# Kernel optimization log

Measured on AMD Instinct MI355X. Metric: run time of the kernel, lower is better.

## Reference

```python
import jax, jax.numpy as jnp
import numpy as np

C = 512
HEADS = 8
HEAD_DIM = C // HEADS
GROUPS = 32
EPS = 1e-5


def group_norm(x, scale, bias):
    b, c, h, w = x.shape
    xg = x.reshape(b, GROUPS, -1)
    mean = xg.mean(axis=-1, keepdims=True)
    var = xg.var(axis=-1, keepdims=True)
    xg = (xg - mean) * jax.lax.rsqrt(var + EPS)
    x = xg.reshape(b, c, h, w)
    return x * scale[None, :, None, None] + bias[None, :, None, None]


def conv1x1(x, w, b):
    # w: (out_c, in_c), x: (B, C, H, W)
    return jnp.einsum('oc,bchw->bohw', w, x) + b[None, :, None, None]


def setup_inputs() -> dict:
    key = jax.random.key(0)
    ks = jax.random.split(key, 11)
    s = 1.0 / np.sqrt(C)
    return {
        'x': jax.random.normal(ks[0], (8, C, 32, 32), jnp.float32),
        'gn_scale': jnp.ones((C,), jnp.float32),
        'gn_bias': jnp.zeros((C,), jnp.float32),
        'wq': jax.random.normal(ks[1], (C, C), jnp.float32) * s,
        'bq': jax.random.normal(ks[2], (C,), jnp.float32) * 0.01,
        'wk': jax.random.normal(ks[3], (C, C), jnp.float32) * s,
        'bk': jax.random.normal(ks[4], (C,), jnp.float32) * 0.01,
        'wv': jax.random.normal(ks[5], (C, C), jnp.float32) * s,
        'bv': jax.random.normal(ks[6], (C,), jnp.float32) * 0.01,
        'wp': jax.random.normal(ks[7], (C, C), jnp.float32) * s,
        'bp': jax.random.normal(ks[8], (C,), jnp.float32) * 0.01,
    }


def reference(x, gn_scale, gn_bias, wq, bq, wk, bk, wv, bv, wp, bp):
    b, c, h, w = x.shape
    n = h * w
    h_in = x
    xn = group_norm(x, gn_scale, gn_bias)
    q = conv1x1(xn, wq, bq).reshape(b, HEADS, HEAD_DIM, n)
    k = conv1x1(xn, wk, bk).reshape(b, HEADS, HEAD_DIM, n)
    v = conv1x1(xn, wv, bv).reshape(b, HEADS, HEAD_DIM, n)
    scale = 1.0 / np.sqrt(HEAD_DIM).astype(np.float32)
    attn = jnp.einsum('bhcn,bhcm->bhnm', q, k) * scale
    attn = jax.nn.softmax(attn, axis=-1)
    out = jnp.einsum('bhnm,bhcm->bhcn', attn, v)
    out = out.reshape(b, c, h, w)
    out = conv1x1(out, wp, bp)
    return out + h_in
```

## Files before the change

kernel.cpp:

```cpp
#include <hip/hip_runtime.h>

#define CC 512
#define NN 1024
#define NB 8
#define NH 8
#define HD 64

typedef __attribute__((ext_vector_type(8))) short s16x8;
typedef __attribute__((ext_vector_type(4))) short s16x4;
typedef __attribute__((ext_vector_type(4))) float f32x4;
typedef __attribute__((ext_vector_type(16))) float f32x16;

__device__ __forceinline__ unsigned cvtpk(float lo, float hi){
  unsigned r;
  asm("v_cvt_pk_bf16_f32 %0, %1, %2" : "=v"(r) : "v"(lo), "v"(hi));
  return r;
}

__device__ __forceinline__ s16x4 pack4(float a, float b, float c, float d){
  union { unsigned u[2]; s16x4 v; } r;
  r.u[0] = cvtpk(a, b);
  r.u[1] = cvtpk(c, d);
  return r.v;
}

__device__ __forceinline__ void gload16(const void* g, void* l){
  __builtin_amdgcn_global_load_lds((const __attribute__((address_space(1))) void*)g,
                                   (__attribute__((address_space(3))) void*)l, 16, 0, 0);
}

__global__ __launch_bounds__(256) void prep_kernel(const float* __restrict__ x,
    const float* __restrict__ gsc, const float* __restrict__ gbi,
    const float* __restrict__ w0, const float* __restrict__ w1,
    const float* __restrict__ w2, const float* __restrict__ w3,
    short* __restrict__ wbf, short* __restrict__ xnt){
  if (blockIdx.x < 1024){
    const int i = blockIdx.x*256 + threadIdx.x;
    const int sel = i >> 16;
    const int off = (i & 65535) << 2;
    const float* src = (sel==0) ? w0 : (sel==1) ? w1 : (sel==2) ? w2 : w3;
    const float4 v = *reinterpret_cast<const float4*>(src + off);
    *reinterpret_cast<s16x4*>(wbf + (size_t)sel*262144 + off) = pack4(v.x, v.y, v.z, v.w);
    return;
  }
  const int blk = blockIdx.x - 1024;
  const int b = blk >> 5;
  const int g = blk & 31;
  const int t = threadIdx.x;
  const float* base = x + ((size_t)b*CC + g*16)*NN;
  float4 vals[16];
  float s = 0.f, s2 = 0.f;
  #pragma unroll
  for (int k = 0; k < 16; ++k){
    float4 v = *reinterpret_cast<const float4*>(base + k*NN + t*4);
    vals[k] = v;
    s  += v.x + v.y + v.z + v.w;
    s2 += v.x*v.x + v.y*v.y + v.z*v.z + v.w*v.w;
  }
  #pragma unroll
  for (int m = 1; m < 64; m <<= 1){ s += __shfl_xor(s, m); s2 += __shfl_xor(s2, m); }
  __shared__ float rs[4], rs2[4];
  const int wid = t >> 6, lane = t & 63;
  if (lane == 0){ rs[wid] = s; rs2[wid] = s2; }
  __syncthreads();
  s  = rs[0] + rs[1] + rs[2] + rs[3];
  s2 = rs2[0] + rs2[1] + rs2[2] + rs2[3];
  const float mean = s * (1.f/16384.f);
  const float inv = rsqrtf(s2 * (1.f/16384.f) - mean*mean + 1e-5f);
  float scl[16], off[16];
  #pragma unroll
  for (int k = 0; k < 16; ++k){
    const float sc = gsc[g*16 + k] * inv;
    scl[k] = sc;
    off[k] = gbi[g*16 + k] - mean * sc;
  }
  short* obase = xnt + ((size_t)b*NN + t*4)*CC + g*16;
  #pragma unroll
  for (int i = 0; i < 4; ++i){
    float fv[16];
    #pragma unroll
    for (int k = 0; k < 16; ++k){
      const float v = (i==0) ? vals[k].x : (i==1) ? vals[k].y : (i==2) ? vals[k].z : vals[k].w;
      fv[k] = v * scl[k] + off[k];
    }
    union { unsigned u[4]; s16x8 v; } lo, hi;
    #pragma unroll
    for (int j = 0; j < 4; ++j){
      lo.u[j] = cvtpk(fv[2*j],     fv[2*j + 1]);
      hi.u[j] = cvtpk(fv[8 + 2*j], fv[8 + 2*j + 1]);
    }
    *reinterpret_cast<s16x8*>(obase + (size_t)i*CC)     = lo.v;
    *reinterpret_cast<s16x8*>(obase + (size_t)i*CC + 8) = hi.v;
  }
}

__global__ __launch_bounds__(256) void gemm_qkv(
    const short* __restrict__ Wb, const short* __restrict__ Bmat,
    const float* __restrict__ bias0, const float* __restrict__ bias1, const float* __restrict__ bias2,
    short* __restrict__ qt, short* __restrict__ kt2, short* __restrict__ vo)
{
  const int w = blockIdx.x;
  const int nt = w & 7;
  const int s = w >> 3;
  const int batch = s & 7;
  const int r = s >> 3;
  const int mt = r & 3, z = r >> 2;
  const int tid = threadIdx.x;
  const int lane = tid & 63, wid = tid >> 6;
  const int wm = wid >> 1, wn = wid & 1;

  __shared__ short As[2][128*32];
  __shared__ short Bs[2][128*32];

  const short* Wz = Wb + (size_t)z * 262144;
  const short* Brow = Bmat + ((size_t)batch*NN + nt*128)*CC;

  const f32x4 fzero = {0.f, 0.f, 0.f, 0.f};
  f32x4 acc[4][4];
  #pragma unroll
  for (int i = 0; i < 4; ++i)
  #pragma unroll
  for (int j = 0; j < 4; ++j)
    acc[i][j] = fzero;

  const int srow = tid >> 2, sh = tid & 3;
  const int sg = sh ^ ((srow >> 1) & 3);
  const short* gaBase = Wz + (size_t)(mt*128 + srow)*CC + sg*8;
  const short* gbBase = Brow + (size_t)srow*CC + sg*8;

  auto stage = [&](int kk, int buf){
    const short* ga = gaBase + kk*32;
    const short* gb = gbBase + kk*32;
    gload16(ga,         &As[buf][tid*8]);
    gload16(ga + 64*CC, &As[buf][(tid + 256)*8]);
    gload16(gb,         &Bs[buf][tid*8]);
    gload16(gb + 64*CC, &Bs[buf][(tid + 256)*8]);
  };

  const int rch = (lane >> 4) ^ (((lane & 15) >> 1) & 3);

  auto compute = [&](int buf){
    s16x8 a[4], b[4];
    #pragma unroll
    for (int mi = 0; mi < 4; ++mi){
      const int row = wm*64 + mi*16 + (lane & 15);
      a[mi] = *reinterpret_cast<const s16x8*>(&As[buf][row*32 + rch*8]);
    }
    #pragma unroll
    for (int ni = 0; ni < 4; ++ni){
      const int row = wn*64 + ni*16 + (lane & 15);
      b[ni] = *reinterpret_cast<const s16x8*>(&Bs[buf][row*32 + rch*8]);
    }
    if (z == 2){
      #pragma unroll
      for (int mi = 0; mi < 4; ++mi)
      #pragma unroll
      for (int ni = 0; ni < 4; ++ni)
        acc[mi][ni] = __builtin_amdgcn_mfma_f32_16x16x32_bf16(b[ni], a[mi], acc[mi][ni], 0, 0, 0);
    } else {
      #pragma unroll
      for (int mi = 0; mi < 4; ++mi)
      #pragma unroll
      for (int ni = 0; ni < 4; ++ni)
        acc[mi][ni] = __builtin_amdgcn_mfma_f32_16x16x32_bf16(a[mi], b[ni], acc[mi][ni], 0, 0, 0);
    }
  };

  stage(0, 0);
  asm volatile("s_waitcnt vmcnt(0)" ::: "memory");
  __builtin_amdgcn_s_barrier();
  int buf = 0;
  #pragma unroll
  for (int kk = 0; kk < 16; ++kk){
    if (kk < 15) stage(kk + 1, buf ^ 1);
    compute(buf);
    if (kk < 15){
      asm volatile("s_waitcnt vmcnt(0)" ::: "memory");
      __builtin_amdgcn_s_barrier();
    }
    buf ^= 1;
  }

  const int obase = mt*128 + wm*64;
  const int head = mt*2 + wm;
  const size_t hb = ((size_t)batch*NH + head)*65536;
  const int hi2 = (lane >> 5) & 1;
  const int j0 = ((lane >> 4) & 1)*4;
  if (z < 2){
    const float* bias = (z == 0) ? bias0 : bias1;
    short* dst = (z == 0) ? qt : kt2;
    const float qs = (z == 0) ? 0.125f * 1.44269504f : 1.0f;
    #pragma unroll
    for (int mi = 0; mi < 4; ++mi){
      float bv4[4];
      #pragma unroll
      for (int r2 = 0; r2 < 4; ++r2) bv4[r2] = bias[obase + mi*16 + (lane>>4)*4 + r2];
      #pragma unroll
      for (int ni = 0; ni < 4; ++ni){
        const int l = (ni & 1)*16 + (lane & 15) + 32*hi2;
        const int q5 = nt*4 + wn*2 + (ni >> 1);
        const s16x4 pk = pack4((acc[mi][ni][0] + bv4[0]) * qs,
                               (acc[mi][ni][1] + bv4[1]) * qs,
                               (acc[mi][ni][2] + bv4[2]) * qs,
                               (acc[mi][ni][3] + bv4[3]) * qs);
        *reinterpret_cast<s16x4*>(dst + hb + (size_t)((q5*4 + mi)*64 + l)*8 + j0) = pk;
      }
    }
  } else {
    #pragma unroll
    for (int mi = 0; mi < 4; ++mi){
      const float bv = bias2[obase + mi*16 + (lane & 15)];
      const int ci = mi >> 1;
      const int cl = (mi & 1)*16 + (lane & 15);
      #pragma unroll
      for (int ni = 0; ni < 4; ++ni){
        const int m5 = nt*2 + wn;
        const s16x4 pk = pack4(acc[mi][ni][0] + bv, acc[mi][ni][1] + bv,
                               acc[mi][ni][2] + bv, acc[mi][ni][3] + bv);
        *reinterpret_cast<s16x4*>(vo + hb + (size_t)((((ci*16 + m5)*4 + ni)*64) + cl + 32*hi2)*8 + j0) = pk;
      }
    }
  }
}

__global__ __launch_bounds__(256) void gemm_proj(
    const short* __restrict__ Wb, const short* __restrict__ Bmat,
    const float* __restrict__ bias0, const float* __restrict__ resid,
    float* __restrict__ outp)
{
  const int w = blockIdx.x;
  const int nt = w & 7;
  const int s = w >> 3;
  const int batch = s & 7;
  const int mt = s >> 3;
  const int tid = threadIdx.x;
  const int lane = tid & 63, wid = tid >> 6;
  const int wm = wid >> 1, wn = wid & 1;

  __shared__ short As[2][128*32];
  __shared__ short Bs[2][128*32];

  const short* Wz = Wb + (size_t)3 * 262144;
  const short* Brow = Bmat + ((size_t)batch*NN + nt*128)*CC;

  const f32x4 fzero = {0.f, 0.f, 0.f, 0.f};
  f32x4 acc[4][4];
  #pragma unroll
  for (int i = 0; i < 4; ++i)
  #pragma unroll
  for (int j = 0; j < 4; ++j)
    acc[i][j] = fzero;

  const int srow = tid >> 2, sh = tid & 3;
  const int sg = sh ^ ((srow >> 1) & 3);
  const short* gaBase = Wz + (size_t)(mt*128 + srow)*CC + sg*8;
  const short* gbBase = Brow + (size_t)srow*CC + sg*8;

  auto stage = [&](int kk, int buf){
    const short* ga = gaBase + kk*32;
    const short* gb = gbBase + kk*32;
    gload16(ga,         &As[buf][tid*8]);
    gload16(ga + 64*CC, &As[buf][(tid + 256)*8]);
    gload16(gb,         &Bs[buf][tid*8]);
    gload16(gb + 64*CC, &Bs[buf][(tid + 256)*8]);
  };

  const int rch = (lane >> 4) ^ (((lane & 15) >> 1) & 3);

  auto compute = [&](int buf){
    s16x8 a[4], b[4];
    #pragma unroll
    for (int mi = 0; mi < 4; ++mi){
      const int row = wm*64 + mi*16 + (lane & 15);
      a[mi] = *reinterpret_cast<const s16x8*>(&As[buf][row*32 + rch*8]);
    }
    #pragma unroll
    for (int ni = 0; ni < 4; ++ni){
      const int row = wn*64 + ni*16 + (lane & 15);
      b[ni] = *reinterpret_cast<const s16x8*>(&Bs[buf][row*32 + rch*8]);
    }
    #pragma unroll
    for (int mi = 0; mi < 4; ++mi)
    #pragma unroll
    for (int ni = 0; ni < 4; ++ni)
      acc[mi][ni] = __builtin_amdgcn_mfma_f32_16x16x32_bf16(b[ni], a[mi], acc[mi][ni], 0, 0, 0);
  };

  stage(0, 0);
  asm volatile("s_waitcnt vmcnt(0)" ::: "memory");
  __builtin_amdgcn_s_barrier();
  int buf = 0;
  #pragma unroll
  for (int kk = 0; kk < 16; ++kk){
    if (kk < 15) stage(kk + 1, buf ^ 1);
    compute(buf);
    if (kk < 15){
      asm volatile("s_waitcnt vmcnt(0)" ::: "memory");
      __builtin_amdgcn_s_barrier();
    }
    buf ^= 1;
  }

  const int obase = mt*128 + wm*64;
  const int nbase = nt*128 + wn*64;
  #pragma unroll
  for (int mi = 0; mi < 4; ++mi){
    const int o = obase + mi*16 + (lane & 15);
    const float bv = bias0[o];
    #pragma unroll
    for (int ni = 0; ni < 4; ++ni){
      const int n4 = nbase + ni*16 + (lane >> 4)*4;
      const size_t idx = ((size_t)batch*CC + o)*NN + n4;
      const float4 rv = *reinterpret_cast<const float4*>(resid + idx);
      float4 ov;
      ov.x = acc[mi][ni][0] + bv + rv.x;
      ov.y = acc[mi][ni][1] + bv + rv.y;
      ov.z = acc[mi][ni][2] + bv + rv.z;
      ov.w = acc[mi][ni][3] + bv + rv.w;
      *reinterpret_cast<float4*>(outp + idx) = ov;
    }
  }
}

__global__ __launch_bounds__(256, 2) void attn_kernel(
    const short* __restrict__ qp, const short* __restrict__ kp, const short* __restrict__ vp,
    short* __restrict__ ot)
{
  const int bid = blockIdx.x;
  const int xcd = bid & 7, slot = bid >> 3;
  const int bh  = xcd*8 + (slot & 7);
  const int qt  = slot >> 3;
  const int b = bh >> 3, head = bh & 7;
  const int tid = threadIdx.x, lane = tid & 63, wid = tid >> 6;
  const int col = lane & 31;

  const short* Qf = qp + (size_t)bh*65536;
  const short* Kf = kp + (size_t)bh*65536;
  const short* Vf = vp + (size_t)bh*65536;

  __shared__ short Ks[2][4096];
  __shared__ short Vs[2][4096];

  const int q5 = qt*4 + wid;
  s16x8 qf[4];
  #pragma unroll
  for (int ks = 0; ks < 4; ++ks)
    qf[ks] = *reinterpret_cast<const s16x8*>(Qf + (size_t)(q5*4 + ks)*512 + lane*8);

  f32x16 of0, of1;
  #pragma unroll
  for (int r = 0; r < 16; ++r){ of0[r] = 0.f; of1[r] = 0.f; }
  float l = 0.f;

  auto stage = [&](int it, int buf){
    gload16(Kf + (size_t)it*4096 + tid*8,        &Ks[buf][tid*8]);
    gload16(Kf + (size_t)it*4096 + 2048 + tid*8, &Ks[buf][2048 + tid*8]);
    gload16(Vf + (size_t)it*2048 + tid*8,        &Vs[buf][tid*8]);
    gload16(Vf + (size_t)(16 + it)*2048 + tid*8, &Vs[buf][2048 + tid*8]);
  };

  auto pack = [&](f32x16& sv, s16x8& p0, s16x8& p1){
    union { unsigned u[4]; s16x8 v; } w0, w1;
    {
      unsigned a = cvtpk(sv[0], sv[1]);
      unsigned c = cvtpk(sv[4], sv[5]);
      auto r = __builtin_amdgcn_permlane32_swap(a, c, false, false);
      w0.u[0] = r[0]; w0.u[2] = r[1];
      a = cvtpk(sv[2], sv[3]);
      c = cvtpk(sv[6], sv[7]);
      r = __builtin_amdgcn_permlane32_swap(a, c, false, false);
      w0.u[1] = r[0]; w0.u[3] = r[1];
    }
    {
      unsigned a = cvtpk(sv[8], sv[9]);
      unsigned c = cvtpk(sv[12], sv[13]);
      auto r = __builtin_amdgcn_permlane32_swap(a, c, false, false);
      w1.u[0] = r[0]; w1.u[2] = r[1];
      a = cvtpk(sv[10], sv[11]);
      c = cvtpk(sv[14], sv[15]);
      r = __builtin_amdgcn_permlane32_swap(a, c, false, false);
      w1.u[1] = r[0]; w1.u[3] = r[1];
    }
    p0 = w0.v; p1 = w1.v;
  };

  auto body = [&](int it, int buf){
    s16x8 kf[2][4];
    #pragma unroll
    for (int t = 0; t < 2; ++t)
      #pragma unroll
      for (int ks = 0; ks < 4; ++ks)
        kf[t][ks] = *reinterpret_cast<const s16x8*>(&Ks[buf][t*2048 + ks*512 + lane*8]);
    if (it < 15) stage(it + 1, buf ^ 1);
    f32x16 s0, s1;
    #pragma unroll
    for (int r = 0; r < 16; ++r){ s0[r] = 0.f; s1[r] = 0.f; }
    #pragma unroll
    for (int ks = 0; ks < 4; ++ks){
      s0 = __builtin_amdgcn_mfma_f32_32x32x16_bf16(kf[0][ks], qf[ks], s0, 0, 0, 0);
      s1 = __builtin_amdgcn_mfma_f32_32x32x16_bf16(kf[1][ks], qf[ks], s1, 0, 0, 0);
    }
    #pragma unroll
    for (int r = 0; r < 16; ++r){ s0[r] = __builtin_amdgcn_exp2f(s0[r]); }
    #pragma unroll
    for (int r = 0; r < 16; ++r){ s1[r] = __builtin_amdgcn_exp2f(s1[r]); }
    float t[16];
    #pragma unroll
    for (int r = 0; r < 16; ++r) t[r] = s0[r] + s1[r];
    #pragma unroll
    for (int o = 8; o > 0; o >>= 1)
      #pragma unroll
      for (int r = 0; r < 8; ++r) if (r < o) t[r] = t[r] + t[r + o];
    l += t[0] + __shfl_xor(t[0], 32);
    s16x8 pf[4];
    pack(s0, pf[0], pf[1]);
    pack(s1, pf[2], pf[3]);
    s16x8 vf[2][4];
    #pragma unroll
    for (int ci = 0; ci < 2; ++ci)
      #pragma unroll
      for (int s = 0; s < 4; ++s)
        vf[ci][s] = *reinterpret_cast<const s16x8*>(&Vs[buf][ci*2048 + s*512 + lane*8]);
    #pragma unroll
    for (int s = 0; s < 4; ++s){
      of0 = __builtin_amdgcn_mfma_f32_32x32x16_bf16(vf[0][s], pf[s], of0, 0, 0, 0);
      of1 = __builtin_amdgcn_mfma_f32_32x32x16_bf16(vf[1][s], pf[s], of1, 0, 0, 0);
    }
    if (it < 15){
      __builtin_amdgcn_sched_barrier(0);
      asm volatile("s_waitcnt vmcnt(0)" ::: "memory");
      __builtin_amdgcn_s_barrier();
    }
  };

  stage(0, 0);
  asm volatile("s_waitcnt vmcnt(0)" ::: "memory");
  __builtin_amdgcn_s_barrier();
  #pragma unroll 1
  for (int ii = 0; ii < 8; ++ii){
    body(2*ii,     0);
    body(2*ii + 1, 1);
  }

  const float linv = 1.f / l;
  const int hi = lane >> 5;
  const int n = qt*128 + wid*32 + col;
  short* ob = ot + ((size_t)b*NN + n)*CC + head*HD + hi*4;
  #pragma unroll
  for (int rq = 0; rq < 4; ++rq){
    s16x4 pk = pack4(of0[rq*4 + 0] * linv, of0[rq*4 + 1] * linv,
                     of0[rq*4 + 2] * linv, of0[rq*4 + 3] * linv);
    *reinterpret_cast<s16x4*>(ob + rq*8) = pk;
    pk = pack4(of1[rq*4 + 0] * linv, of1[rq*4 + 1] * linv,
               of1[rq*4 + 2] * linv, of1[rq*4 + 3] * linv);
    *reinterpret_cast<s16x4*>(ob + 32 + rq*8) = pk;
  }
}

extern "C" void kernel_launch(void* const* d_in, const int* in_sizes, int n_in,
                              void* d_out, int out_size, void* d_ws, size_t ws_size,
                              hipStream_t stream) {
  const float* x   = (const float*)d_in[0];
  const float* gsc = (const float*)d_in[1];
  const float* gbi = (const float*)d_in[2];
  const float* wq  = (const float*)d_in[3];
  const float* bq  = (const float*)d_in[4];
  const float* wk  = (const float*)d_in[5];
  const float* bk  = (const float*)d_in[6];
  const float* wv  = (const float*)d_in[7];
  const float* bv  = (const float*)d_in[8];
  const float* wp  = (const float*)d_in[9];
  const float* bp  = (const float*)d_in[10];
  float* out = (float*)d_out;

  char* ws = (char*)d_ws;
  short* wbf = (short*)(ws);
  short* xnt = (short*)(ws + (2u<<20));
  short* qt  = (short*)(ws + (10u<<20));
  short* kt  = (short*)(ws + (18u<<20));
  short* v   = (short*)(ws + (26u<<20));
  short* aot = (short*)(ws + (34u<<20));

  prep_kernel<<<1280, 256, 0, stream>>>(x, gsc, gbi, wq, wk, wv, wp, wbf, xnt);
  gemm_qkv<<<dim3(768), 256, 0, stream>>>(wbf, xnt, bq, bk, bv, qt, kt, v);
  attn_kernel<<<dim3(512), 256, 0, stream>>>(qt, kt, v, aot);
  gemm_proj<<<dim3(256), 256, 0, stream>>>(wbf, aot, bp, x, out);
}
```

Before: 74.52 us.

## Split attention KV loop across two wave groups per block and merge partials

```diff
diff --git a/kernel.cpp b/kernel.cpp
--- a/kernel.cpp
+++ b/kernel.cpp
@@ -322,7 +322,7 @@
   }
 }
 
-__global__ __launch_bounds__(256, 2) void attn_kernel(
+__global__ __launch_bounds__(512, 2) void attn_kernel(
     const short* __restrict__ qp, const short* __restrict__ kp, const short* __restrict__ vp,
     short* __restrict__ ot)
 {
@@ -333,15 +333,15 @@
   const int b = bh >> 3, head = bh & 7;
   const int tid = threadIdx.x, lane = tid & 63, wid = tid >> 6;
   const int col = lane & 31;
+  const int kh = wid >> 2, qw = wid & 3;
 
   const short* Qf = qp + (size_t)bh*65536;
   const short* Kf = kp + (size_t)bh*65536;
   const short* Vf = vp + (size_t)bh*65536;
 
-  __shared__ short Ks[2][4096];
-  __shared__ short Vs[2][4096];
-
-  const int q5 = qt*4 + wid;
+  __shared__ short smem[32768];
+
+  const int q5 = qt*4 + qw;
   s16x8 qf[4];
   #pragma unroll
   for (int ks = 0; ks < 4; ++ks)
@@ -352,11 +352,15 @@
   for (int r = 0; r < 16; ++r){ of0[r] = 0.f; of1[r] = 0.f; }
   float l = 0.f;
 
+  const int sth = tid >> 8, st = tid & 255;
   auto stage = [&](int it, int buf){
-    gload16(Kf + (size_t)it*4096 + tid*8,        &Ks[buf][tid*8]);
-    gload16(Kf + (size_t)it*4096 + 2048 + tid*8, &Ks[buf][2048 + tid*8]);
-    gload16(Vf + (size_t)it*2048 + tid*8,        &Vs[buf][tid*8]);
-    gload16(Vf + (size_t)(16 + it)*2048 + tid*8, &Vs[buf][2048 + tid*8]);
+    const int tk = sth*8 + it;
+    short* Kd = smem + buf*8192 + sth*4096;
+    short* Vd = smem + 16384 + buf*8192 + sth*4096;
+    gload16(Kf + (size_t)tk*4096 + st*8,        Kd + st*8);
+    gload16(Kf + (size_t)tk*4096 + 2048 + st*8, Kd + 2048 + st*8);
+    gload16(Vf + (size_t)tk*2048 + st*8,        Vd + st*8);
+    gload16(Vf + (size_t)(16 + tk)*2048 + st*8, Vd + 2048 + st*8);
   };
 
   auto pack = [&](f32x16& sv, s16x8& p0, s16x8& p1){
@@ -385,13 +389,15 @@
   };
 
   auto body = [&](int it, int buf){
+    const short* Kb = smem + buf*8192 + kh*4096;
+    const short* Vb = smem + 16384 + buf*8192 + kh*4096;
     s16x8 kf[2][4];
     #pragma unroll
     for (int t = 0; t < 2; ++t)
       #pragma unroll
       for (int ks = 0; ks < 4; ++ks)
-        kf[t][ks] = *reinterpret_cast<const s16x8*>(&Ks[buf][t*2048 + ks*512 + lane*8]);
-    if (it < 15) stage(it + 1, buf ^ 1);
+        kf[t][ks] = *reinterpret_cast<const s16x8*>(Kb + t*2048 + ks*512 + lane*8);
+    if (it < 7) stage(it + 1, buf ^ 1);
     f32x16 s0, s1;
     #pragma unroll
     for (int r = 0; r < 16; ++r){ s0[r] = 0.f; s1[r] = 0.f; }
@@ -420,13 +426,13 @@
     for (int ci = 0; ci < 2; ++ci)
       #pragma unroll
       for (int s = 0; s < 4; ++s)
-        vf[ci][s] = *reinterpret_cast<const s16x8*>(&Vs[buf][ci*2048 + s*512 + lane*8]);
+        vf[ci][s] = *reinterpret_cast<const s16x8*>(Vb + ci*2048 + s*512 + lane*8);
     #pragma unroll
     for (int s = 0; s < 4; ++s){
       of0 = __builtin_amdgcn_mfma_f32_32x32x16_bf16(vf[0][s], pf[s], of0, 0, 0, 0);
       of1 = __builtin_amdgcn_mfma_f32_32x32x16_bf16(vf[1][s], pf[s], of1, 0, 0, 0);
     }
-    if (it < 15){
+    if (it < 7){
       __builtin_amdgcn_sched_barrier(0);
       asm volatile("s_waitcnt vmcnt(0)" ::: "memory");
       __builtin_amdgcn_s_barrier();
@@ -437,23 +443,40 @@
   asm volatile("s_waitcnt vmcnt(0)" ::: "memory");
   __builtin_amdgcn_s_barrier();
   #pragma unroll 1
-  for (int ii = 0; ii < 8; ++ii){
+  for (int ii = 0; ii < 4; ++ii){
     body(2*ii,     0);
     body(2*ii + 1, 1);
   }
 
-  const float linv = 1.f / l;
-  const int hi = lane >> 5;
-  const int n = qt*128 + wid*32 + col;
-  short* ob = ot + ((size_t)b*NN + n)*CC + head*HD + hi*4;
-  #pragma unroll
-  for (int rq = 0; rq < 4; ++rq){
-    s16x4 pk = pack4(of0[rq*4 + 0] * linv, of0[rq*4 + 1] * linv,
-                     of0[rq*4 + 2] * linv, of0[rq*4 + 3] * linv);
-    *reinterpret_cast<s16x4*>(ob + rq*8) = pk;
-    pk = pack4(of1[rq*4 + 0] * linv, of1[rq*4 + 1] * linv,
-               of1[rq*4 + 2] * linv, of1[rq*4 + 3] * linv);
-    *reinterpret_cast<s16x4*>(ob + 32 + rq*8) = pk;
+  __syncthreads();
+  float* Lf = reinterpret_cast<float*>(smem);
+  if (kh == 1){
+    #pragma unroll
+    for (int r = 0; r < 16; ++r){
+      Lf[(qw*32 + r)*64 + lane]      = of0[r];
+      Lf[(qw*32 + 16 + r)*64 + lane] = of1[r];
+    }
+    Lf[8192 + qw*64 + lane] = l;
+  }
+  __syncthreads();
+  if (kh == 0){
+    const float linv = 1.f / (l + Lf[8192 + qw*64 + lane]);
+    const int hi = lane >> 5;
+    const int n = qt*128 + qw*32 + col;
+    short* ob = ot + ((size_t)b*NN + n)*CC + head*HD + hi*4;
+    #pragma unroll
+    for (int rq = 0; rq < 4; ++rq){
+      s16x4 pk = pack4((of0[rq*4 + 0] + Lf[(qw*32 + rq*4 + 0)*64 + lane]) * linv,
+                       (of0[rq*4 + 1] + Lf[(qw*32 + rq*4 + 1)*64 + lane]) * linv,
+                       (of0[rq*4 + 2] + Lf[(qw*32 + rq*4 + 2)*64 + lane]) * linv,
+                       (of0[rq*4 + 3] + Lf[(qw*32 + rq*4 + 3)*64 + lane]) * linv);
+      *reinterpret_cast<s16x4*>(ob + rq*8) = pk;
+      pk = pack4((of1[rq*4 + 0] + Lf[(qw*32 + 16 + rq*4 + 0)*64 + lane]) * linv,
+                 (of1[rq*4 + 1] + Lf[(qw*32 + 16 + rq*4 + 1)*64 + lane]) * linv,
+                 (of1[rq*4 + 2] + Lf[(qw*32 + 16 + rq*4 + 2)*64 + lane]) * linv,
+                 (of1[rq*4 + 3] + Lf[(qw*32 + 16 + rq*4 + 3)*64 + lane]) * linv);
+      *reinterpret_cast<s16x4*>(ob + 32 + rq*8) = pk;
+    }
   }
 }
 
@@ -483,6 +506,6 @@
 
   prep_kernel<<<1280, 256, 0, stream>>>(x, gsc, gbi, wq, wk, wv, wp, wbf, xnt);
   gemm_qkv<<<dim3(768), 256, 0, stream>>>(wbf, xnt, bq, bk, bv, qt, kt, v);
-  attn_kernel<<<dim3(512), 256, 0, stream>>>(qt, kt, v, aot);
+  attn_kernel<<<dim3(512), 512, 0, stream>>>(qt, kt, v, aot);
   gemm_proj<<<dim3(256), 256, 0, stream>>>(wbf, aot, bp, x, out);
 }
```

Result: no change. 75.67 us (+1.5%).

## Software-pipeline attention loop: overlap QK MFMA of next tile with softmax/PV of previous

Applied to the files above, without the earlier changes.

```diff
diff --git a/kernel.cpp b/kernel.cpp
--- a/kernel.cpp
+++ b/kernel.cpp
@@ -384,63 +384,85 @@
     p0 = w0.v; p1 = w1.v;
   };
 
-  auto body = [&](int it, int buf){
+  f32x16 sp0, sp1, sc0, sc1;
+  s16x8 vprev[2][4], vcur[2][4];
+
+  auto front = [&](int it, int buf){
     s16x8 kf[2][4];
     #pragma unroll
     for (int t = 0; t < 2; ++t)
       #pragma unroll
       for (int ks = 0; ks < 4; ++ks)
         kf[t][ks] = *reinterpret_cast<const s16x8*>(&Ks[buf][t*2048 + ks*512 + lane*8]);
+    #pragma unroll
+    for (int ci = 0; ci < 2; ++ci)
+      #pragma unroll
+      for (int s = 0; s < 4; ++s)
+        vcur[ci][s] = *reinterpret_cast<const s16x8*>(&Vs[buf][ci*2048 + s*512 + lane*8]);
     if (it < 15) stage(it + 1, buf ^ 1);
-    f32x16 s0, s1;
-    #pragma unroll
-    for (int r = 0; r < 16; ++r){ s0[r] = 0.f; s1[r] = 0.f; }
+    #pragma unroll
+    for (int r = 0; r < 16; ++r){ sc0[r] = 0.f; sc1[r] = 0.f; }
     #pragma unroll
     for (int ks = 0; ks < 4; ++ks){
-      s0 = __builtin_amdgcn_mfma_f32_32x32x16_bf16(kf[0][ks], qf[ks], s0, 0, 0, 0);
-      s1 = __builtin_amdgcn_mfma_f32_32x32x16_bf16(kf[1][ks], qf[ks], s1, 0, 0, 0);
-    }
-    #pragma unroll
-    for (int r = 0; r < 16; ++r){ s0[r] = __builtin_amdgcn_exp2f(s0[r]); }
-    #pragma unroll
-    for (int r = 0; r < 16; ++r){ s1[r] = __builtin_amdgcn_exp2f(s1[r]); }
+      sc0 = __builtin_amdgcn_mfma_f32_32x32x16_bf16(kf[0][ks], qf[ks], sc0, 0, 0, 0);
+      sc1 = __builtin_amdgcn_mfma_f32_32x32x16_bf16(kf[1][ks], qf[ks], sc1, 0, 0, 0);
+    }
+  };
+
+  auto back = [&](){
+    #pragma unroll
+    for (int r = 0; r < 16; ++r){ sp0[r] = __builtin_amdgcn_exp2f(sp0[r]); }
+    #pragma unroll
+    for (int r = 0; r < 16; ++r){ sp1[r] = __builtin_amdgcn_exp2f(sp1[r]); }
     float t[16];
     #pragma unroll
-    for (int r = 0; r < 16; ++r) t[r] = s0[r] + s1[r];
+    for (int r = 0; r < 16; ++r) t[r] = sp0[r] + sp1[r];
     #pragma unroll
     for (int o = 8; o > 0; o >>= 1)
       #pragma unroll
       for (int r = 0; r < 8; ++r) if (r < o) t[r] = t[r] + t[r + o];
     l += t[0] + __shfl_xor(t[0], 32);
     s16x8 pf[4];
-    pack(s0, pf[0], pf[1]);
-    pack(s1, pf[2], pf[3]);
-    s16x8 vf[2][4];
+    pack(sp0, pf[0], pf[1]);
+    pack(sp1, pf[2], pf[3]);
+    #pragma unroll
+    for (int s = 0; s < 4; ++s){
+      of0 = __builtin_amdgcn_mfma_f32_32x32x16_bf16(vprev[0][s], pf[s], of0, 0, 0, 0);
+      of1 = __builtin_amdgcn_mfma_f32_32x32x16_bf16(vprev[1][s], pf[s], of1, 0, 0, 0);
+    }
+  };
+
+  auto shift = [&](){
+    sp0 = sc0; sp1 = sc1;
     #pragma unroll
     for (int ci = 0; ci < 2; ++ci)
       #pragma unroll
       for (int s = 0; s < 4; ++s)
-        vf[ci][s] = *reinterpret_cast<const s16x8*>(&Vs[buf][ci*2048 + s*512 + lane*8]);
-    #pragma unroll
-    for (int s = 0; s < 4; ++s){
-      of0 = __builtin_amdgcn_mfma_f32_32x32x16_bf16(vf[0][s], pf[s], of0, 0, 0, 0);
-      of1 = __builtin_amdgcn_mfma_f32_32x32x16_bf16(vf[1][s], pf[s], of1, 0, 0, 0);
-    }
-    if (it < 15){
-      __builtin_amdgcn_sched_barrier(0);
-      asm volatile("s_waitcnt vmcnt(0)" ::: "memory");
-      __builtin_amdgcn_s_barrier();
-    }
+        vprev[ci][s] = vcur[ci][s];
   };
 
   stage(0, 0);
   asm volatile("s_waitcnt vmcnt(0)" ::: "memory");
   __builtin_amdgcn_s_barrier();
+
+  front(0, 0); shift();
+  __builtin_amdgcn_sched_barrier(0);
+  asm volatile("s_waitcnt vmcnt(0)" ::: "memory");
+  __builtin_amdgcn_s_barrier();
+
   #pragma unroll 1
-  for (int ii = 0; ii < 8; ++ii){
-    body(2*ii,     0);
-    body(2*ii + 1, 1);
-  }
+  for (int ii = 0; ii < 7; ++ii){
+    front(2*ii + 1, 1); back(); shift();
+    __builtin_amdgcn_sched_barrier(0);
+    asm volatile("s_waitcnt vmcnt(0)" ::: "memory");
+    __builtin_amdgcn_s_barrier();
+    front(2*ii + 2, 0); back(); shift();
+    __builtin_amdgcn_sched_barrier(0);
+    asm volatile("s_waitcnt vmcnt(0)" ::: "memory");
+    __builtin_amdgcn_s_barrier();
+  }
+  front(15, 1); back(); shift();
+  back();
 
   const float linv = 1.f / l;
   const int hi = lane >> 5;
```

After: 74.53 us. Within noise of the previous version (+0.0%).
